# Kernel tuning notes

Measured on AMD Instinct MI355X. Metric: run time of the kernel, lower is better.

Reference implementation:

```python
import jax, jax.numpy as jnp
import numpy as np

L = 128          # bandlimit (max_l)
NTHETA = 256     # Gauss-Legendre latitudes (>= L for exact quadrature)
NPHI = 512       # longitudes (>= 2L-1)
C_IN, C_OUT = 32, 32


def _normalized_assoc_legendre(Lmax, xg):
    """Pbar_lm(x) with Condon-Shortley phase, orthonormal on the sphere.
    Returns (Lmax, Lmax, T) for m>=0; zero for m>l."""
    T = xg.shape[0]
    P = np.zeros((Lmax, Lmax, T), dtype=np.float64)
    sx = np.sqrt(np.maximum(1.0 - xg * xg, 0.0))
    P[0, 0] = 1.0 / np.sqrt(4.0 * np.pi)
    for m in range(1, Lmax):
        P[m, m] = -np.sqrt((2 * m + 1) / (2.0 * m)) * sx * P[m - 1, m - 1]
    for m in range(0, Lmax - 1):
        P[m + 1, m] = np.sqrt(2 * m + 3.0) * xg * P[m, m]
    for m in range(Lmax):
        for l in range(m + 2, Lmax):
            a = np.sqrt((4.0 * l * l - 1.0) / (l * l - m * m))
            b = np.sqrt(((l - 1.0) ** 2 - m * m) / (4.0 * (l - 1.0) ** 2 - 1.0))
            P[l, m] = a * (xg * P[l - 1, m] - b * P[l - 2, m])
    return P


def _build_basis():
    # Gauss-Legendre quadrature in cos(theta): exact for degree <= 2*NTHETA-1
    xg, wg = np.polynomial.legendre.leggauss(NTHETA)
    P = _normalized_assoc_legendre(L, xg)  # (L, L, T), m>=0
    # Full basis B[l, m+L-1, t]; Pbar_{l,-m} = (-1)^m Pbar_{l,m}
    B = np.zeros((L, 2 * L - 1, NTHETA), dtype=np.float64)
    for m in range(-(L - 1), L):
        B[:, m + L - 1, :] = ((-1.0) ** abs(m) if m < 0 else 1.0) * P[:, abs(m), :]
    return B.astype(np.float32), wg.astype(np.float32)


def setup_inputs() -> dict:
    key = jax.random.key(0)
    k1, k2, k3 = jax.random.split(key, 3)
    x = jax.random.normal(k1, (NTHETA, NPHI, C_IN), dtype=jnp.float32)
    std = 1.0 / (C_IN + C_OUT)
    wr = std * jax.random.normal(k2, (L, 2 * L - 1, C_IN, C_OUT), dtype=jnp.float32)
    wi = std * jax.random.normal(k3, (L, 2 * L - 1, C_IN, C_OUT), dtype=jnp.float32)
    B, wg = _build_basis()
    return {"x": x, "weights_real": wr, "weights_imag": wi,
            "legendre": jnp.asarray(B), "quad_w": jnp.asarray(wg)}


def reference(x, weights_real, weights_imag, legendre, quad_w):
    ntheta, nphi, _ = x.shape
    Lb = legendre.shape[0]
    # --- forward SHT (per channel, vectorized) ---
    # longitude FFT: Fm[t,k,c] = sum_p x e^{-i 2pi k p / nphi}; dphi = 2pi/nphi
    Fm = jnp.fft.fft(x.astype(jnp.complex64), axis=1) * (2.0 * np.pi / nphi)
    midx = np.arange(-(Lb - 1), Lb) % nphi            # FFT bins for m=-(L-1)..L-1
    Fm_sel = Fm[:, midx, :]                           # (t, 2L-1, c)
    Bw = legendre * quad_w[None, None, :]             # quadrature-weighted basis
    # flm[l,m,c] = sum_t w_t Pbar_lm(theta_t) Fm[t,m,c]
    flm = jnp.einsum('lmt,tmc->lmc', Bw.astype(jnp.complex64), Fm_sel)
    # --- spectral conv: per-(l,m) channel mixing ---
    W = weights_real.astype(jnp.complex64) + 1j * weights_imag.astype(jnp.complex64)
    y = jnp.einsum('lmc,lmco->lmo', flm, W)           # (L, 2L-1, O)
    # --- inverse SHT ---
    G = jnp.einsum('lmt,lmo->tmo', legendre.astype(jnp.complex64), y)  # (t, 2L-1, O)
    spec = jnp.zeros((ntheta, nphi, G.shape[-1]), dtype=jnp.complex64)
    spec = spec.at[:, midx, :].set(G)
    out = jnp.fft.ifft(spec, axis=1) * nphi           # f = sum_m G e^{i m phi}
    return jnp.moveaxis(out.real, 2, 0)               # (O, ntheta, nphi)
```

## Files before the change

kernel.cpp:

```cpp
#include <hip/hip_runtime.h>
#include <math.h>

#define DEVFN __global__ __launch_bounds__(256)

namespace {
constexpr int LL  = 128;
constexpr int MM2 = 255;
constexpr int NT  = 256;
constexpr int NP  = 512;
constexpr int NC  = 32;
constexpr int NO  = 32;
constexpr float TWO_PI = 6.283185307179586476925286766559f;
}

typedef short v8s __attribute__((ext_vector_type(8)));
typedef float v4f __attribute__((ext_vector_type(4)));

__device__ inline unsigned short f2bf(float f) {
  unsigned int u = __float_as_uint(f);
  return (unsigned short)((u + 0x7FFFu + ((u >> 16) & 1u)) >> 16);
}

__device__ inline int m_of(int k, int mloc) {
  return (mloc < 8) ? (8 * k + mloc) : (120 - 8 * k + (mloc - 8));
}

DEVFN void kp_prep(const float* __restrict__ x, unsigned short* __restrict__ tw1t,
                   unsigned short* __restrict__ vt, unsigned short* __restrict__ xb) {
  __shared__ float sm[32][65];
  const int bid = blockIdx.x;
  const int tid = threadIdx.x;
  const float phi = TWO_PI / (float)NP;
  if (bid < 512) {
    const int idx = bid * 256 + tid;
    const float fs = TWO_PI / (float)NP;
    {
      const int n = idx >> 9, p = idx & 511;
      const int m = n >> 1;
      const int k = (m * p) & (NP - 1);
      float s, c;
      sincosf(phi * (float)k, &s, &c);
      tw1t[idx] = f2bf((n & 1) ? (-s * fs) : (c * fs));
    }
    {
      const int p = idx >> 8, k = idx & 255;
      const int m = k >> 1;
      const int kk = (m * p) & (NP - 1);
      float s, c;
      sincosf(phi * (float)kk, &s, &c);
      vt[idx] = f2bf((k & 1) ? s : c);
    }
  } else {
    const int q = bid - 512;
    const int t = q >> 3;
    const int p0 = (q & 7) * 64;
#pragma unroll
    for (int i = 0; i < 8; ++i) {
      const int idx = tid + i * 256;
      const int p = idx >> 5, c = idx & 31;
      sm[c][p] = x[((size_t)t * NP + p0 + p) * NC + c];
    }
    __syncthreads();
    const int c = tid >> 3, pg = tid & 7;
    unsigned short pk[8];
#pragma unroll
    for (int u = 0; u < 8; ++u) pk[u] = f2bf(sm[c][pg * 8 + u]);
    *(uint4*)(xb + ((size_t)(t * 32 + c)) * NP + p0 + pg * 8) = *(const uint4*)pk;
  }
}

DEVFN void k1_mfma(const unsigned short* __restrict__ xb,
                   const unsigned short* __restrict__ tw1t,
                   const float* __restrict__ wg,
                   float* __restrict__ fwr, float* __restrict__ fwi) {
  __shared__ unsigned short As[128 * 32];
  __shared__ unsigned short Bs[64 * 32];
  const int tid = threadIdx.x;
  const int r0 = blockIdx.x * 128;
  const int n0 = blockIdx.y * 64;
  const int wid = tid >> 6, lane = tid & 63;
  const int wm = wid & 1, wn = wid >> 1;
  v4f acc[4][2];
#pragma unroll
  for (int i = 0; i < 4; ++i)
#pragma unroll
    for (int j = 0; j < 2; ++j) {
      acc[i][j][0] = 0.f; acc[i][j][1] = 0.f; acc[i][j][2] = 0.f; acc[i][j][3] = 0.f;
    }
  const int lr = lane & 15, lk = (lane >> 4) * 8;
  for (int k0 = 0; k0 < 512; k0 += 32) {
#pragma unroll
    for (int s = 0; s < 3; ++s) {
      const int chunk = tid + s * 256;
      if (chunk < 512) {
        const int row = chunk >> 2, c16 = chunk & 3;
        *(uint4*)&As[row * 32 + c16 * 8] =
            *(const uint4*)&xb[(size_t)(r0 + row) * 512 + k0 + c16 * 8];
      } else {
        const int bc = chunk - 512;
        const int row = bc >> 2, c16 = bc & 3;
        *(uint4*)&Bs[row * 32 + c16 * 8] =
            *(const uint4*)&tw1t[(size_t)(n0 + row) * 512 + k0 + c16 * 8];
      }
    }
    __syncthreads();
    v8s af[4], bf[2];
#pragma unroll
    for (int i = 0; i < 4; ++i) af[i] = *(const v8s*)&As[(wm * 64 + i * 16 + lr) * 32 + lk];
#pragma unroll
    for (int j = 0; j < 2; ++j) bf[j] = *(const v8s*)&Bs[(wn * 32 + j * 16 + lr) * 32 + lk];
#pragma unroll
    for (int i = 0; i < 4; ++i)
#pragma unroll
      for (int j = 0; j < 2; ++j)
        acc[i][j] = __builtin_amdgcn_mfma_f32_16x16x32_bf16(af[i], bf[j], acc[i][j], 0, 0, 0);
    __syncthreads();
  }
  const int lrow = (lane >> 4) * 4;
#pragma unroll
  for (int i = 0; i < 4; ++i) {
    const int rbase = r0 + wm * 64 + i * 16 + lrow;
    const int t = rbase >> 5, c0 = rbase & 31;
    const float w = wg[t];
#pragma unroll
    for (int j = 0; j < 2; ++j) {
      const int n = n0 + wn * 32 + j * 16 + lr;
      const int mI = n >> 1;
      float* dst = (n & 1) ? fwi : fwr;
      float4 v = {acc[i][j][0] * w, acc[i][j][1] * w, acc[i][j][2] * w, acc[i][j][3] * w};
      *(float4*)&dst[((size_t)mI * NT + t) * NC + c0] = v;
    }
  }
}

DEVFN void k2_flm(const float* __restrict__ leg, const float* __restrict__ fwr,
                  const float* __restrict__ fwi, float* __restrict__ flr,
                  float* __restrict__ fli) {
  const int m  = blockIdx.x;
  const int l0 = m + blockIdx.y * 8 + (threadIdx.x >> 6) * 2;
  if (l0 >= LL) return;
  const int lane = threadIdx.x & 63;
  const int c = lane & 31;
  const int l1 = min(l0 + 1, LL - 1);
  const float* fp = ((lane >> 5) ? fwi : fwr) + (size_t)m * NT * NC + c;
  const float* lgA = leg + ((size_t)(l0 * MM2 + 127 + m)) * NT;
  const float* lgB = leg + ((size_t)(l1 * MM2 + 127 + m)) * NT;
  float a0 = 0.f, a1 = 0.f;
#pragma unroll 4
  for (int t = 0; t < NT; t += 4) {
    const float f0 = fp[(t + 0) * NC];
    const float f1 = fp[(t + 1) * NC];
    const float f2 = fp[(t + 2) * NC];
    const float f3 = fp[(t + 3) * NC];
    const float4 bA = *(const float4*)(lgA + t);
    const float4 bB = *(const float4*)(lgB + t);
    a0 = fmaf(bA.x, f0, a0); a0 = fmaf(bA.y, f1, a0);
    a0 = fmaf(bA.z, f2, a0); a0 = fmaf(bA.w, f3, a0);
    a1 = fmaf(bB.x, f0, a1); a1 = fmaf(bB.y, f1, a1);
    a1 = fmaf(bB.z, f2, a1); a1 = fmaf(bB.w, f3, a1);
  }
  float* outp = (lane >> 5) ? fli : flr;
  outp[(size_t)(m * LL + l0) * NC + c] = a0;
  if (l0 + 1 < LL) outp[(size_t)(m * LL + l0 + 1) * NC + c] = a1;
}

DEVFN void k3_mix(const float* __restrict__ flr, const float* __restrict__ fli,
                  const float* __restrict__ wr, const float* __restrict__ wi,
                  float* __restrict__ ya, float* __restrict__ yb) {
  const int m  = blockIdx.x;
  const int wid = threadIdx.x >> 6, lane = threadIdx.x & 63;
  const int l = m + blockIdx.y * 4 + wid;
  if (l >= LL) return;
  const int c8 = lane >> 3;
  const int o8 = lane & 7;
  const int c0 = c8 * 4, o0 = o8 * 4;
  const float s0 = (m > 0) ? 1.0f : 0.0f;
  const size_t rp = ((size_t)(l * MM2 + 127 + m) * NC) * NO;
  const size_t rn = ((size_t)(l * MM2 + 127 - m) * NC) * NO;
  const float4 fa4 = *(const float4*)&flr[(size_t)(m * LL + l) * NC + c0];
  const float4 fb4 = *(const float4*)&fli[(size_t)(m * LL + l) * NC + c0];
  float4 accA = {0.f, 0.f, 0.f, 0.f}, accB = {0.f, 0.f, 0.f, 0.f};
#pragma unroll
  for (int i = 0; i < 4; ++i) {
    const int c = c0 + i;
    const float4 wrp = *(const float4*)&wr[rp + (size_t)c * NO + o0];
    const float4 wrn = *(const float4*)&wr[rn + (size_t)c * NO + o0];
    const float4 wip = *(const float4*)&wi[rp + (size_t)c * NO + o0];
    const float4 win = *(const float4*)&wi[rn + (size_t)c * NO + o0];
    const float fa = (i == 0) ? fa4.x : (i == 1) ? fa4.y : (i == 2) ? fa4.z : fa4.w;
    const float fb = (i == 0) ? fb4.x : (i == 1) ? fb4.y : (i == 2) ? fb4.z : fb4.w;
    float4 wa, wb;
    wa.x = fmaf(s0, wrn.x, wrp.x); wa.y = fmaf(s0, wrn.y, wrp.y);
    wa.z = fmaf(s0, wrn.z, wrp.z); wa.w = fmaf(s0, wrn.w, wrp.w);
    wb.x = fmaf(s0, win.x, -wip.x); wb.y = fmaf(s0, win.y, -wip.y);
    wb.z = fmaf(s0, win.z, -wip.z); wb.w = fmaf(s0, win.w, -wip.w);
    accA.x = fmaf(fa, wa.x, fmaf(fb, wb.x, accA.x));
    accA.y = fmaf(fa, wa.y, fmaf(fb, wb.y, accA.y));
    accA.z = fmaf(fa, wa.z, fmaf(fb, wb.z, accA.z));
    accA.w = fmaf(fa, wa.w, fmaf(fb, wb.w, accA.w));
    accB.x = fmaf(fa, wb.x, fmaf(-fb, wa.x, accB.x));
    accB.y = fmaf(fa, wb.y, fmaf(-fb, wa.y, accB.y));
    accB.z = fmaf(fa, wb.z, fmaf(-fb, wa.z, accB.z));
    accB.w = fmaf(fa, wb.w, fmaf(-fb, wa.w, accB.w));
  }
#pragma unroll
  for (int mask = 8; mask <= 32; mask <<= 1) {
    accA.x += __shfl_xor(accA.x, mask); accA.y += __shfl_xor(accA.y, mask);
    accA.z += __shfl_xor(accA.z, mask); accA.w += __shfl_xor(accA.w, mask);
    accB.x += __shfl_xor(accB.x, mask); accB.y += __shfl_xor(accB.y, mask);
    accB.z += __shfl_xor(accB.z, mask); accB.w += __shfl_xor(accB.w, mask);
  }
  if (c8 == 0) {
    *(float4*)&ya[(size_t)(m * LL + l) * NO + o0] = accA;
    *(float4*)&yb[(size_t)(m * LL + l) * NO + o0] = accB;
  }
}

DEVFN void k4_G(const float* __restrict__ leg, const float* __restrict__ ya,
                const float* __restrict__ yb, unsigned short* __restrict__ ut) {
  const int fid = blockIdx.x + (int)blockIdx.y * 128;
  const int xk  = fid & 7;
  const int loc = fid >> 3;
  const int m   = m_of(xk, loc >> 3);
  const int tc  = loc & 7;
  const int o = threadIdx.x & 31;
  const int tq = threadIdx.x >> 5;
  const int t0 = tc * 32 + tq * 4;
  float aa[4] = {}, bb[4] = {};
#pragma unroll 4
  for (int l = m; l < LL; ++l) {
    const float4 g = *(const float4*)(leg + ((size_t)(l * MM2 + 127 + m)) * NT + t0);
    const float yav = ya[(m * LL + l) * NO + o];
    const float ybv = yb[(m * LL + l) * NO + o];
    aa[0] = fmaf(g.x, yav, aa[0]);  bb[0] = fmaf(g.x, ybv, bb[0]);
    aa[1] = fmaf(g.y, yav, aa[1]);  bb[1] = fmaf(g.y, ybv, bb[1]);
    aa[2] = fmaf(g.z, yav, aa[2]);  bb[2] = fmaf(g.z, ybv, bb[2]);
    aa[3] = fmaf(g.w, yav, aa[3]);  bb[3] = fmaf(g.w, ybv, bb[3]);
  }
#pragma unroll
  for (int i = 0; i < 4; ++i) {
    const unsigned int pk = (unsigned int)f2bf(aa[i]) | ((unsigned int)f2bf(bb[i]) << 16);
    *(unsigned int*)&ut[((size_t)((t0 + i) * 32 + o)) * 256 + 2 * m] = pk;
  }
}

DEVFN void k5_mfma(const unsigned short* __restrict__ ut,
                   const unsigned short* __restrict__ vt,
                   float* __restrict__ out) {
  __shared__ unsigned short As[128 * 32];
  __shared__ unsigned short Bs[128 * 32];
  const int tid = threadIdx.x;
  const int p0 = blockIdx.x * 128;
  const int r0 = blockIdx.y * 128;
  const int wid = tid >> 6, lane = tid & 63;
  const int wm = wid & 1, wn = wid >> 1;
  v4f acc[4][4];
#pragma unroll
  for (int i = 0; i < 4; ++i)
#pragma unroll
    for (int j = 0; j < 4; ++j) {
      acc[i][j][0] = 0.f; acc[i][j][1] = 0.f; acc[i][j][2] = 0.f; acc[i][j][3] = 0.f;
    }
  const int lr = lane & 15, lk = (lane >> 4) * 8;
  for (int k0 = 0; k0 < 256; k0 += 32) {
#pragma unroll
    for (int s = 0; s < 2; ++s) {
      const int chunk = tid + s * 256;
      const int row = chunk >> 2, c16 = chunk & 3;
      *(uint4*)&As[row * 32 + c16 * 8] =
          *(const uint4*)&vt[(size_t)(p0 + row) * 256 + k0 + c16 * 8];
      *(uint4*)&Bs[row * 32 + c16 * 8] =
          *(const uint4*)&ut[(size_t)(r0 + row) * 256 + k0 + c16 * 8];
    }
    __syncthreads();
    v8s af[4], bf[4];
#pragma unroll
    for (int i = 0; i < 4; ++i) af[i] = *(const v8s*)&As[(wm * 64 + i * 16 + lr) * 32 + lk];
#pragma unroll
    for (int j = 0; j < 4; ++j) bf[j] = *(const v8s*)&Bs[(wn * 64 + j * 16 + lr) * 32 + lk];
#pragma unroll
    for (int i = 0; i < 4; ++i)
#pragma unroll
      for (int j = 0; j < 4; ++j)
        acc[i][j] = __builtin_amdgcn_mfma_f32_16x16x32_bf16(af[i], bf[j], acc[i][j], 0, 0, 0);
    __syncthreads();
  }
  const int lrow = (lane >> 4) * 4;
#pragma unroll
  for (int i = 0; i < 4; ++i) {
    const int pbase = p0 + wm * 64 + i * 16 + lrow;
#pragma unroll
    for (int j = 0; j < 4; ++j) {
      const int r = r0 + wn * 64 + j * 16 + lr;
      const int t = r >> 5, o = r & 31;
      float4 v = {acc[i][j][0], acc[i][j][1], acc[i][j][2], acc[i][j][3]};
      *(float4*)&out[((size_t)o * NT + t) * NP + pbase] = v;
    }
  }
}

extern "C" void kernel_launch(void* const* d_in, const int* in_sizes, int n_in,
                              void* d_out, int out_size, void* d_ws, size_t ws_size,
                              hipStream_t stream) {
  const float* x   = (const float*)d_in[0];
  const float* wr  = (const float*)d_in[1];
  const float* wi  = (const float*)d_in[2];
  const float* leg = (const float*)d_in[3];
  const float* wg  = (const float*)d_in[4];
  float* out = (float*)d_out;

  unsigned short* tw1t = (unsigned short*)d_ws;
  unsigned short* vt   = tw1t + 131072;
  unsigned short* xb   = vt + 131072;
  unsigned short* ut   = xb + 4194304;
  float* fwr = (float*)(ut + 2097152);
  float* fwi = fwr + 1048576;
  float* flr = fwi + 1048576;
  float* fli = flr + 524288;
  float* ya  = fli + 524288;
  float* yb  = ya + 524288;

  hipLaunchKernelGGL(kp_prep, dim3(2560), dim3(256), 0, stream, x, tw1t, vt, xb);
  hipLaunchKernelGGL(k1_mfma, dim3(64, 4), dim3(256), 0, stream, xb, tw1t, wg, fwr, fwi);
  hipLaunchKernelGGL(k2_flm, dim3(128, 16), dim3(256), 0, stream, leg, fwr, fwi, flr, fli);
  hipLaunchKernelGGL(k3_mix, dim3(128, 32), dim3(256), 0, stream, flr, fli, wr, wi, ya, yb);
  hipLaunchKernelGGL(k4_G, dim3(128, 8), dim3(256), 0, stream, leg, ya, yb, ut);
  hipLaunchKernelGGL(k5_mfma, dim3(4, 64), dim3(256), 0, stream, ut, vt, out);
}
```

Before: 364.8 us.

## Retile GEMM kernels, widen Legendre reuse, hoist weight loads, simplify k4 mapping

Halves the row tile of both MFMA GEMM kernels to launch more blocks, and adds a launch-bounds occupancy hint to every kernel except kp_prep. The forward Legendre kernel now has each wave compute four degrees instead of two, reusing each Fm load across more outputs. The mixing kernel issues all weight loads up front. The inverse Legendre kernel drops its interleaved m-to-block mapping in favour of a direct one and unrolls deeper. Smaller GEMM tiles mean less data reuse per block in exchange for better load balance, and dropping the interleaved mapping may worsen balance across the triangular l range.

```diff
diff --git a/kernel.cpp b/kernel.cpp
--- a/kernel.cpp
+++ b/kernel.cpp
@@ -2,6 +2,7 @@
 #include <math.h>
 
 #define DEVFN __global__ __launch_bounds__(256)
+#define DEVFN4 __global__ __launch_bounds__(256, 4)
 
 namespace {
 constexpr int LL  = 128;
@@ -19,10 +20,6 @@
 __device__ inline unsigned short f2bf(float f) {
   unsigned int u = __float_as_uint(f);
   return (unsigned short)((u + 0x7FFFu + ((u >> 16) & 1u)) >> 16);
-}
-
-__device__ inline int m_of(int k, int mloc) {
-  return (mloc < 8) ? (8 * k + mloc) : (120 - 8 * k + (mloc - 8));
 }
 
 DEVFN void kp_prep(const float* __restrict__ x, unsigned short* __restrict__ tw1t,
@@ -69,48 +66,37 @@
   }
 }
 
-DEVFN void k1_mfma(const unsigned short* __restrict__ xb,
-                   const unsigned short* __restrict__ tw1t,
-                   const float* __restrict__ wg,
-                   float* __restrict__ fwr, float* __restrict__ fwi) {
-  __shared__ unsigned short As[128 * 32];
+DEVFN4 void k1_mfma(const unsigned short* __restrict__ xb,
+                    const unsigned short* __restrict__ tw1t,
+                    const float* __restrict__ wg,
+                    float* __restrict__ fwr, float* __restrict__ fwi) {
+  __shared__ unsigned short As[64 * 32];
   __shared__ unsigned short Bs[64 * 32];
   const int tid = threadIdx.x;
-  const int r0 = blockIdx.x * 128;
+  const int r0 = blockIdx.x * 64;
   const int n0 = blockIdx.y * 64;
   const int wid = tid >> 6, lane = tid & 63;
   const int wm = wid & 1, wn = wid >> 1;
-  v4f acc[4][2];
-#pragma unroll
-  for (int i = 0; i < 4; ++i)
-#pragma unroll
-    for (int j = 0; j < 2; ++j) {
-      acc[i][j][0] = 0.f; acc[i][j][1] = 0.f; acc[i][j][2] = 0.f; acc[i][j][3] = 0.f;
-    }
+  v4f acc[2][2];
+#pragma unroll
+  for (int i = 0; i < 2; ++i)
+#pragma unroll
+    for (int j = 0; j < 2; ++j) acc[i][j] = (v4f){0.f, 0.f, 0.f, 0.f};
   const int lr = lane & 15, lk = (lane >> 4) * 8;
+  const int row = tid >> 2, c16 = tid & 3;
   for (int k0 = 0; k0 < 512; k0 += 32) {
-#pragma unroll
-    for (int s = 0; s < 3; ++s) {
-      const int chunk = tid + s * 256;
-      if (chunk < 512) {
-        const int row = chunk >> 2, c16 = chunk & 3;
-        *(uint4*)&As[row * 32 + c16 * 8] =
-            *(const uint4*)&xb[(size_t)(r0 + row) * 512 + k0 + c16 * 8];
-      } else {
-        const int bc = chunk - 512;
-        const int row = bc >> 2, c16 = bc & 3;
-        *(uint4*)&Bs[row * 32 + c16 * 8] =
-            *(const uint4*)&tw1t[(size_t)(n0 + row) * 512 + k0 + c16 * 8];
-      }
-    }
-    __syncthreads();
-    v8s af[4], bf[2];
-#pragma unroll
-    for (int i = 0; i < 4; ++i) af[i] = *(const v8s*)&As[(wm * 64 + i * 16 + lr) * 32 + lk];
+    *(uint4*)&As[row * 32 + c16 * 8] =
+        *(const uint4*)&xb[(size_t)(r0 + row) * 512 + k0 + c16 * 8];
+    *(uint4*)&Bs[row * 32 + c16 * 8] =
+        *(const uint4*)&tw1t[(size_t)(n0 + row) * 512 + k0 + c16 * 8];
+    __syncthreads();
+    v8s af[2], bf[2];
+#pragma unroll
+    for (int i = 0; i < 2; ++i) af[i] = *(const v8s*)&As[(wm * 32 + i * 16 + lr) * 32 + lk];
 #pragma unroll
     for (int j = 0; j < 2; ++j) bf[j] = *(const v8s*)&Bs[(wn * 32 + j * 16 + lr) * 32 + lk];
 #pragma unroll
-    for (int i = 0; i < 4; ++i)
+    for (int i = 0; i < 2; ++i)
 #pragma unroll
       for (int j = 0; j < 2; ++j)
         acc[i][j] = __builtin_amdgcn_mfma_f32_16x16x32_bf16(af[i], bf[j], acc[i][j], 0, 0, 0);
@@ -118,8 +104,8 @@
   }
   const int lrow = (lane >> 4) * 4;
 #pragma unroll
-  for (int i = 0; i < 4; ++i) {
-    const int rbase = r0 + wm * 64 + i * 16 + lrow;
+  for (int i = 0; i < 2; ++i) {
+    const int rbase = r0 + wm * 32 + i * 16 + lrow;
     const int t = rbase >> 5, c0 = rbase & 31;
     const float w = wg[t];
 #pragma unroll
@@ -133,41 +119,47 @@
   }
 }
 
-DEVFN void k2_flm(const float* __restrict__ leg, const float* __restrict__ fwr,
-                  const float* __restrict__ fwi, float* __restrict__ flr,
-                  float* __restrict__ fli) {
-  const int m  = blockIdx.x;
-  const int l0 = m + blockIdx.y * 8 + (threadIdx.x >> 6) * 2;
-  if (l0 >= LL) return;
-  const int lane = threadIdx.x & 63;
+DEVFN4 void k2_flm(const float* __restrict__ leg, const float* __restrict__ fwr,
+                   const float* __restrict__ fwi, float* __restrict__ flr,
+                   float* __restrict__ fli) {
+  const int m = blockIdx.x;
+  const int wid = threadIdx.x >> 6, lane = threadIdx.x & 63;
+  const int lb = m + blockIdx.y * 16 + wid * 4;
+  if (lb >= LL) return;
   const int c = lane & 31;
-  const int l1 = min(l0 + 1, LL - 1);
   const float* fp = ((lane >> 5) ? fwi : fwr) + (size_t)m * NT * NC + c;
-  const float* lgA = leg + ((size_t)(l0 * MM2 + 127 + m)) * NT;
-  const float* lgB = leg + ((size_t)(l1 * MM2 + 127 + m)) * NT;
-  float a0 = 0.f, a1 = 0.f;
-#pragma unroll 4
+  const float* lg[4];
+#pragma unroll
+  for (int i = 0; i < 4; ++i) {
+    const int l = min(lb + i, LL - 1);
+    lg[i] = leg + ((size_t)(l * MM2 + 127 + m)) * NT;
+  }
+  float a[4] = {};
+#pragma unroll 2
   for (int t = 0; t < NT; t += 4) {
     const float f0 = fp[(t + 0) * NC];
     const float f1 = fp[(t + 1) * NC];
     const float f2 = fp[(t + 2) * NC];
     const float f3 = fp[(t + 3) * NC];
-    const float4 bA = *(const float4*)(lgA + t);
-    const float4 bB = *(const float4*)(lgB + t);
-    a0 = fmaf(bA.x, f0, a0); a0 = fmaf(bA.y, f1, a0);
-    a0 = fmaf(bA.z, f2, a0); a0 = fmaf(bA.w, f3, a0);
-    a1 = fmaf(bB.x, f0, a1); a1 = fmaf(bB.y, f1, a1);
-    a1 = fmaf(bB.z, f2, a1); a1 = fmaf(bB.w, f3, a1);
+#pragma unroll
+    for (int i = 0; i < 4; ++i) {
+      const float4 b = *(const float4*)(lg[i] + t);
+      a[i] = fmaf(b.x, f0, a[i]);
+      a[i] = fmaf(b.y, f1, a[i]);
+      a[i] = fmaf(b.z, f2, a[i]);
+      a[i] = fmaf(b.w, f3, a[i]);
+    }
   }
   float* outp = (lane >> 5) ? fli : flr;
-  outp[(size_t)(m * LL + l0) * NC + c] = a0;
-  if (l0 + 1 < LL) outp[(size_t)(m * LL + l0 + 1) * NC + c] = a1;
-}
-
-DEVFN void k3_mix(const float* __restrict__ flr, const float* __restrict__ fli,
-                  const float* __restrict__ wr, const float* __restrict__ wi,
-                  float* __restrict__ ya, float* __restrict__ yb) {
-  const int m  = blockIdx.x;
+#pragma unroll
+  for (int i = 0; i < 4; ++i)
+    if (lb + i < LL) outp[(size_t)(m * LL + lb + i) * NC + c] = a[i];
+}
+
+DEVFN4 void k3_mix(const float* __restrict__ flr, const float* __restrict__ fli,
+                   const float* __restrict__ wr, const float* __restrict__ wi,
+                   float* __restrict__ ya, float* __restrict__ yb) {
+  const int m = blockIdx.x;
   const int wid = threadIdx.x >> 6, lane = threadIdx.x & 63;
   const int l = m + blockIdx.y * 4 + wid;
   if (l >= LL) return;
@@ -177,23 +169,27 @@
   const float s0 = (m > 0) ? 1.0f : 0.0f;
   const size_t rp = ((size_t)(l * MM2 + 127 + m) * NC) * NO;
   const size_t rn = ((size_t)(l * MM2 + 127 - m) * NC) * NO;
+  float4 Wrp[4], Wrn[4], Wip[4], Win[4];
+#pragma unroll
+  for (int i = 0; i < 4; ++i) {
+    const size_t co = (size_t)(c0 + i) * NO + o0;
+    Wrp[i] = *(const float4*)&wr[rp + co];
+    Wrn[i] = *(const float4*)&wr[rn + co];
+    Wip[i] = *(const float4*)&wi[rp + co];
+    Win[i] = *(const float4*)&wi[rn + co];
+  }
   const float4 fa4 = *(const float4*)&flr[(size_t)(m * LL + l) * NC + c0];
   const float4 fb4 = *(const float4*)&fli[(size_t)(m * LL + l) * NC + c0];
   float4 accA = {0.f, 0.f, 0.f, 0.f}, accB = {0.f, 0.f, 0.f, 0.f};
 #pragma unroll
   for (int i = 0; i < 4; ++i) {
-    const int c = c0 + i;
-    const float4 wrp = *(const float4*)&wr[rp + (size_t)c * NO + o0];
-    const float4 wrn = *(const float4*)&wr[rn + (size_t)c * NO + o0];
-    const float4 wip = *(const float4*)&wi[rp + (size_t)c * NO + o0];
-    const float4 win = *(const float4*)&wi[rn + (size_t)c * NO + o0];
     const float fa = (i == 0) ? fa4.x : (i == 1) ? fa4.y : (i == 2) ? fa4.z : fa4.w;
     const float fb = (i == 0) ? fb4.x : (i == 1) ? fb4.y : (i == 2) ? fb4.z : fb4.w;
     float4 wa, wb;
-    wa.x = fmaf(s0, wrn.x, wrp.x); wa.y = fmaf(s0, wrn.y, wrp.y);
-    wa.z = fmaf(s0, wrn.z, wrp.z); wa.w = fmaf(s0, wrn.w, wrp.w);
-    wb.x = fmaf(s0, win.x, -wip.x); wb.y = fmaf(s0, win.y, -wip.y);
-    wb.z = fmaf(s0, win.z, -wip.z); wb.w = fmaf(s0, win.w, -wip.w);
+    wa.x = fmaf(s0, Wrn[i].x, Wrp[i].x); wa.y = fmaf(s0, Wrn[i].y, Wrp[i].y);
+    wa.z = fmaf(s0, Wrn[i].z, Wrp[i].z); wa.w = fmaf(s0, Wrn[i].w, Wrp[i].w);
+    wb.x = fmaf(s0, Win[i].x, -Wip[i].x); wb.y = fmaf(s0, Win[i].y, -Wip[i].y);
+    wb.z = fmaf(s0, Win[i].z, -Wip[i].z); wb.w = fmaf(s0, Win[i].w, -Wip[i].w);
     accA.x = fmaf(fa, wa.x, fmaf(fb, wb.x, accA.x));
     accA.y = fmaf(fa, wa.y, fmaf(fb, wb.y, accA.y));
     accA.z = fmaf(fa, wa.z, fmaf(fb, wb.z, accA.z));
@@ -216,18 +212,15 @@
   }
 }
 
-DEVFN void k4_G(const float* __restrict__ leg, const float* __restrict__ ya,
-                const float* __restrict__ yb, unsigned short* __restrict__ ut) {
-  const int fid = blockIdx.x + (int)blockIdx.y * 128;
-  const int xk  = fid & 7;
-  const int loc = fid >> 3;
-  const int m   = m_of(xk, loc >> 3);
-  const int tc  = loc & 7;
+DEVFN4 void k4_G(const float* __restrict__ leg, const float* __restrict__ ya,
+                 const float* __restrict__ yb, unsigned short* __restrict__ ut) {
+  const int m = blockIdx.x;
+  const int tc = blockIdx.y;
   const int o = threadIdx.x & 31;
   const int tq = threadIdx.x >> 5;
   const int t0 = tc * 32 + tq * 4;
   float aa[4] = {}, bb[4] = {};
-#pragma unroll 4
+#pragma unroll 8
   for (int l = m; l < LL; ++l) {
     const float4 g = *(const float4*)(leg + ((size_t)(l * MM2 + 127 + m)) * NT + t0);
     const float yav = ya[(m * LL + l) * NO + o];
@@ -244,54 +237,56 @@
   }
 }
 
-DEVFN void k5_mfma(const unsigned short* __restrict__ ut,
-                   const unsigned short* __restrict__ vt,
-                   float* __restrict__ out) {
-  __shared__ unsigned short As[128 * 32];
+DEVFN4 void k5_mfma(const unsigned short* __restrict__ ut,
+                    const unsigned short* __restrict__ vt,
+                    float* __restrict__ out) {
+  __shared__ unsigned short As[64 * 32];
   __shared__ unsigned short Bs[128 * 32];
   const int tid = threadIdx.x;
-  const int p0 = blockIdx.x * 128;
+  const int p0 = blockIdx.x * 64;
   const int r0 = blockIdx.y * 128;
   const int wid = tid >> 6, lane = tid & 63;
-  const int wm = wid & 1, wn = wid >> 1;
-  v4f acc[4][4];
+  v4f acc[4][2];
 #pragma unroll
   for (int i = 0; i < 4; ++i)
 #pragma unroll
-    for (int j = 0; j < 4; ++j) {
-      acc[i][j][0] = 0.f; acc[i][j][1] = 0.f; acc[i][j][2] = 0.f; acc[i][j][3] = 0.f;
-    }
+    for (int j = 0; j < 2; ++j) acc[i][j] = (v4f){0.f, 0.f, 0.f, 0.f};
   const int lr = lane & 15, lk = (lane >> 4) * 8;
   for (int k0 = 0; k0 < 256; k0 += 32) {
 #pragma unroll
-    for (int s = 0; s < 2; ++s) {
+    for (int s = 0; s < 3; ++s) {
       const int chunk = tid + s * 256;
-      const int row = chunk >> 2, c16 = chunk & 3;
-      *(uint4*)&As[row * 32 + c16 * 8] =
-          *(const uint4*)&vt[(size_t)(p0 + row) * 256 + k0 + c16 * 8];
-      *(uint4*)&Bs[row * 32 + c16 * 8] =
-          *(const uint4*)&ut[(size_t)(r0 + row) * 256 + k0 + c16 * 8];
-    }
-    __syncthreads();
-    v8s af[4], bf[4];
-#pragma unroll
-    for (int i = 0; i < 4; ++i) af[i] = *(const v8s*)&As[(wm * 64 + i * 16 + lr) * 32 + lk];
-#pragma unroll
-    for (int j = 0; j < 4; ++j) bf[j] = *(const v8s*)&Bs[(wn * 64 + j * 16 + lr) * 32 + lk];
+      if (chunk < 256) {
+        const int row = chunk >> 2, c16 = chunk & 3;
+        *(uint4*)&As[row * 32 + c16 * 8] =
+            *(const uint4*)&vt[(size_t)(p0 + row) * 256 + k0 + c16 * 8];
+      } else {
+        const int bc = chunk - 256;
+        const int row = bc >> 2, c16 = bc & 3;
+        *(uint4*)&Bs[row * 32 + c16 * 8] =
+            *(const uint4*)&ut[(size_t)(r0 + row) * 256 + k0 + c16 * 8];
+      }
+    }
+    __syncthreads();
+    v8s af[4], bf[2];
+#pragma unroll
+    for (int i = 0; i < 4; ++i) af[i] = *(const v8s*)&As[(i * 16 + lr) * 32 + lk];
+#pragma unroll
+    for (int j = 0; j < 2; ++j) bf[j] = *(const v8s*)&Bs[(wid * 32 + j * 16 + lr) * 32 + lk];
 #pragma unroll
     for (int i = 0; i < 4; ++i)
 #pragma unroll
-      for (int j = 0; j < 4; ++j)
+      for (int j = 0; j < 2; ++j)
         acc[i][j] = __builtin_amdgcn_mfma_f32_16x16x32_bf16(af[i], bf[j], acc[i][j], 0, 0, 0);
     __syncthreads();
   }
   const int lrow = (lane >> 4) * 4;
 #pragma unroll
   for (int i = 0; i < 4; ++i) {
-    const int pbase = p0 + wm * 64 + i * 16 + lrow;
-#pragma unroll
-    for (int j = 0; j < 4; ++j) {
-      const int r = r0 + wn * 64 + j * 16 + lr;
+    const int pbase = p0 + i * 16 + lrow;
+#pragma unroll
+    for (int j = 0; j < 2; ++j) {
+      const int r = r0 + wid * 32 + j * 16 + lr;
       const int t = r >> 5, o = r & 31;
       float4 v = {acc[i][j][0], acc[i][j][1], acc[i][j][2], acc[i][j][3]};
       *(float4*)&out[((size_t)o * NT + t) * NP + pbase] = v;
@@ -321,9 +316,9 @@
   float* yb  = ya + 524288;
 
   hipLaunchKernelGGL(kp_prep, dim3(2560), dim3(256), 0, stream, x, tw1t, vt, xb);
-  hipLaunchKernelGGL(k1_mfma, dim3(64, 4), dim3(256), 0, stream, xb, tw1t, wg, fwr, fwi);
-  hipLaunchKernelGGL(k2_flm, dim3(128, 16), dim3(256), 0, stream, leg, fwr, fwi, flr, fli);
+  hipLaunchKernelGGL(k1_mfma, dim3(128, 4), dim3(256), 0, stream, xb, tw1t, wg, fwr, fwi);
+  hipLaunchKernelGGL(k2_flm, dim3(128, 8), dim3(256), 0, stream, leg, fwr, fwi, flr, fli);
   hipLaunchKernelGGL(k3_mix, dim3(128, 32), dim3(256), 0, stream, flr, fli, wr, wi, ya, yb);
   hipLaunchKernelGGL(k4_G, dim3(128, 8), dim3(256), 0, stream, leg, ya, yb, ut);
-  hipLaunchKernelGGL(k5_mfma, dim3(4, 64), dim3(256), 0, stream, ut, vt, out);
-}
+  hipLaunchKernelGGL(k5_mfma, dim3(8, 64), dim3(256), 0, stream, ut, vt, out);
+}
```

New measurement: 379.3 us. 4.0% more time.
